# Performance work log

Measured on AMD Instinct MI355X. Metric: run time of the kernel, lower is better.

## Reference

```python
import jax, jax.numpy as jnp
import numpy as np

EPS = 0.01       # l2-normalize epsilon
BN_EPS = 0.001   # batchnorm epsilon

def _l2norm(u):
    # tf.math.l2_normalize over axis=-2: x / sqrt(max(sum(x^2), eps))
    sq = jnp.sum(u * u, axis=-2, keepdims=True)
    return u / jnp.sqrt(jnp.maximum(sq, EPS))

def _dotprod(t, u):
    # einsum '...ij,...ik->...jk' contracting spatial axis, then flatten (C,C)->C*C
    d = jnp.einsum('bndi,bndj->bnij', t, _l2norm(u))
    return d.reshape(d.shape[0], d.shape[1], -1)

def _bn(x, gamma, beta):
    # inference-mode BN with moving_mean=0, moving_var=1 (fresh init)
    return gamma * (x / jnp.sqrt(1.0 + BN_EPS)) + beta

def setup_inputs() -> dict:
    key = jax.random.key(0)
    ks = jax.random.split(key, 9)
    B, N, D, C, BAS, U_IN, U_EQ = 8, 1024, 3, 64, 16, 512, 64
    F = 2 * C * C  # 8192 invariant features (2 input heads)
    t1 = jax.random.normal(ks[0], (B, N, D, C), dtype=jnp.float32)
    t2 = jax.random.normal(ks[1], (B, N, D, C), dtype=jnp.float32)
    u1 = jax.random.normal(ks[2], (B, N, D, C), dtype=jnp.float32)
    u2 = jax.random.normal(ks[3], (B, N, D, C), dtype=jnp.float32)
    V1 = jax.random.normal(ks[4], (B, N, D, BAS), dtype=jnp.float32)
    V2 = jax.random.normal(ks[5], (B, N, D, BAS), dtype=jnp.float32)
    W_inv = jax.random.normal(ks[6], (F, U_IN), dtype=jnp.float32) * 0.02
    b_inv = jnp.zeros((U_IN,), dtype=jnp.float32)
    g_inv = jnp.ones((U_IN,), dtype=jnp.float32)
    be_inv = jnp.zeros((U_IN,), dtype=jnp.float32)
    # two equivariant heads, each Dense(units=U_EQ*BAS)
    W_eq = jax.random.normal(ks[7], (2, F, U_EQ * BAS), dtype=jnp.float32) * 0.02
    b_eq = jnp.zeros((2, U_EQ * BAS), dtype=jnp.float32)
    g_eq = jnp.ones((2, U_EQ * BAS), dtype=jnp.float32)
    be_eq = jnp.zeros((2, U_EQ * BAS), dtype=jnp.float32)
    return {"t1": t1, "t2": t2, "u1": u1, "u2": u2, "V1": V1, "V2": V2,
            "W_inv": W_inv, "b_inv": b_inv, "g_inv": g_inv, "be_inv": be_inv,
            "W_eq": W_eq, "b_eq": b_eq, "g_eq": g_eq, "be_eq": be_eq}

def reference(t1, t2, u1, u2, V1, V2, W_inv, b_inv, g_inv, be_inv,
              W_eq, b_eq, g_eq, be_eq):
    # invariant features: concatenated flattened Gram blocks of the two heads
    feats = jnp.concatenate([_dotprod(t1, u1), _dotprod(t2, u2)], axis=-1)  # (B,N,F)
    # invariant branch: Dense -> BN -> ReLU
    invar = jax.nn.relu(_bn(feats @ W_inv + b_inv, g_inv, be_inv))  # (B,N,U_IN)
    # equivariant branch per head: Dense -> BN -> ReLU -> reshape -> basis recombine
    bas = V1.shape[-1]
    u_eq = W_eq.shape[-1] // bas
    eq_outs = []
    for l, V in enumerate((V1, V2)):
        wl = jax.nn.relu(_bn(feats @ W_eq[l] + b_eq[l], g_eq[l], be_eq[l]))
        wl = wl.reshape(wl.shape[0], wl.shape[1], u_eq, bas)  # (B,N,units,basis)
        # einsum '...ij,...mj->...mi': combine basis vectors -> (B,N,3,units)
        eq_outs.append(jnp.einsum('bnij,bnmj->bnmi', wl, V))
    eqvar = jnp.concatenate(eq_outs, axis=-1)  # (B,N,3,2*units)
    return invar, eqvar
```

## Files before the change

### kernel.cpp

```cpp
#include <hip/hip_runtime.h>
#include <hip/hip_bf16.h>

#define BROWS 8192
#define DDIM 3
#define CDIM 64
#define KF 8192
#define NINV 512
#define NEQ 1024
#define NTOT 2560
#define BAS 16
#define UEQ 64


typedef float f32x4 __attribute__((ext_vector_type(4)));
typedef __bf16 bf16x8_t __attribute__((ext_vector_type(8)));
typedef __bf16 bf16x4_t __attribute__((ext_vector_type(4)));

__device__ __forceinline__ void async_copy16(const void* g, void* l) {
    __builtin_amdgcn_global_load_lds(
        (__attribute__((address_space(1))) void*)(g),
        (__attribute__((address_space(3))) void*)(l), 16, 0, 0);
}

#define FROWS 16
#define FSTRIDE 196

__global__ __launch_bounds__(256) void feats_kernel(
    const float* __restrict__ t1, const float* __restrict__ t2,
    const float* __restrict__ u1, const float* __restrict__ u2,
    __hip_bfloat16* __restrict__ feats)
{
    __shared__ float sT1[FROWS * FSTRIDE];
    __shared__ float sT2[FROWS * FSTRIDE];
    __shared__ float sU1[FROWS * FSTRIDE];
    __shared__ float sU2[FROWS * FSTRIDE];

    const int tid = threadIdx.x;
    const int r0  = blockIdx.x * FROWS;

    #pragma unroll
    for (int k = 0; k < 12; ++k) {
        const int item = k * 256 + tid;
        const int r = item / 192, c = item - r * 192;
        const size_t g = (size_t)(r0 + r) * 192 + c;
        const int l = r * FSTRIDE + c;
        sT1[l] = t1[g];
        sT2[l] = t2[g];
        sU1[l] = u1[g];
        sU2[l] = u2[g];
    }
    __syncthreads();

    #pragma unroll
    for (int k = 0; k < 8; ++k) {
        const int item = k * 256 + tid;
        const int r = item >> 7, rem = item & 127;
        const int h = rem >> 6, c = rem & 63;
        float* U = (h ? sU2 : sU1) + r * FSTRIDE;
        float sq = U[c] * U[c] + U[64 + c] * U[64 + c] + U[128 + c] * U[128 + c];
        float s = 1.0f / sqrtf(fmaxf(sq, 0.01f));
        U[c] *= s; U[64 + c] *= s; U[128 + c] *= s;
    }
    __syncthreads();

    const int w       = tid >> 6;
    const int lane    = tid & 63;
    const int r_local = lane >> 2;
    const int p       = lane & 3;
    const int mb      = r0 >> 8;
    const int rloc0   = r0 & 255;
    const int rloc    = rloc0 + r_local;
    const int lc      = (p - (rloc >> 1)) & 3;
    const float* Tarr = (w >= 2 ? sT2 : sT1) + r_local * FSTRIDE;
    const float* Uarr = (w >= 2 ? sU2 : sU1) + r_local * FSTRIDE;

    char* dst = (char*)feats + (((size_t)(mb * 256 + w * 64)) << 14)
              + rloc0 * 64 + lane * 16;

    #pragma unroll 4
    for (int it = 0; it < 64; ++it) {
        const int kt = w * 64 + it;
        const int i  = (kt >> 1) & 63;
        const int jh = (kt & 1) * 32;
        const int j0 = jh + lc * 8;
        const float ti0 = Tarr[i], ti1 = Tarr[64 + i], ti2 = Tarr[128 + i];
        bf16x8_t vv;
        #pragma unroll
        for (int half = 0; half < 2; ++half) {
            const int j = j0 + half * 4;
            const float4 u0 = *reinterpret_cast<const float4*>(Uarr + j);
            const float4 u1_ = *reinterpret_cast<const float4*>(Uarr + 64 + j);
            const float4 u2_ = *reinterpret_cast<const float4*>(Uarr + 128 + j);
            vv[half * 4 + 0] = (__bf16)(ti0 * u0.x + ti1 * u1_.x + ti2 * u2_.x);
            vv[half * 4 + 1] = (__bf16)(ti0 * u0.y + ti1 * u1_.y + ti2 * u2_.y);
            vv[half * 4 + 2] = (__bf16)(ti0 * u0.z + ti1 * u1_.z + ti2 * u2_.z);
            vv[half * 4 + 3] = (__bf16)(ti0 * u0.w + ti1 * u1_.w + ti2 * u2_.w);
        }
        *reinterpret_cast<bf16x8_t*>(dst) = vv;
        dst += 16384;
    }
}

__global__ __launch_bounds__(256) void wt_kernel(
    const float* __restrict__ W_inv, const float* __restrict__ W_eq,
    __hip_bfloat16* __restrict__ WT)
{
    __shared__ float tile[64][33];
    const int tid = threadIdx.x;
    const int n0 = blockIdx.x * 32;
    const int k0 = blockIdx.y * 64;

    const float* src; int ldn, nl0;
    if (n0 < NINV)            { src = W_inv;                       ldn = NINV; nl0 = n0; }
    else if (n0 < NINV + NEQ) { src = W_eq;                        ldn = NEQ;  nl0 = n0 - NINV; }
    else                      { src = W_eq + (size_t)KF * NEQ;     ldn = NEQ;  nl0 = n0 - NINV - NEQ; }

    {
        const int tx = tid & 31;
        const int ty = tid >> 5;
        #pragma unroll
        for (int i = 0; i < 8; ++i) {
            const int kl = ty + i * 8;
            tile[kl][tx] = src[(size_t)(k0 + kl) * ldn + nl0 + tx];
        }
    }
    __syncthreads();

    const int kt_l = tid >> 7;
    const int rem  = tid & 127;
    const int n_l  = rem >> 2;
    const int p    = rem & 3;

    const int n    = n0 + n_l;
    const int nb   = n / 320, rloc = n - nb * 320;
    const int kt_g = (k0 >> 5) + kt_l;
    const int lc   = (p - (rloc >> 1)) & 3;

    bf16x8_t v;
    #pragma unroll
    for (int e = 0; e < 8; ++e)
        v[e] = (__bf16)tile[kt_l * 32 + lc * 8 + e][n_l];

    char* dst = (char*)WT + ((size_t)(nb * 256 + kt_g)) * 20480
              + rloc * 64 + p * 16;
    *reinterpret_cast<bf16x8_t*>(dst) = v;
}

#define BM 128
#define BN 160
#define BK 32
#define ATILE 16384
#define BTILE 20480
#define AHALF 8192
#define BHALF 10240

__global__ __launch_bounds__(512, 4) void gemm_kernel(
    const __hip_bfloat16* __restrict__ A,
    const __hip_bfloat16* __restrict__ BT,
    const float* __restrict__ b_inv, const float* __restrict__ g_inv,
    const float* __restrict__ be_inv,
    const float* __restrict__ b_eq,  const float* __restrict__ g_eq,
    const float* __restrict__ be_eq,
    float* __restrict__ out_inv,
    float* __restrict__ Yeq)
{
    __shared__ alignas(16) __hip_bfloat16 AsBuf[4][BM * BK];
    __shared__ alignas(16) __hip_bfloat16 BsBuf[4][BN * BK];

    const int tid  = threadIdx.x;
    const int wave = tid >> 6;
    const int lane = tid & 63;
    const bool loWave = wave < 2;

    const int b    = blockIdx.x;
    const int xcd  = b & 7;
    const int slot = b >> 3;
    const int N    = slot & 15;
    const int M    = xcd * 8 + (slot >> 4);
    const int n0   = N * BN;
    const int m0   = M * BM;

    const char* pA = (const char*)A  + (size_t)(M >> 1) * 256 * ATILE
                   + (size_t)(M & 1) * AHALF;
    const char* pB = (const char*)BT + (size_t)(N >> 1) * 256 * BTILE
                   + (size_t)(N & 1) * BHALF;

    const int off16 = tid * 16;

    const int chnk = (((lane >> 4) + ((lane & 15) >> 1)) & 3) * 8;
    const int wm = (wave & 3) * 32;
    const int wn = (wave >> 2) * 80;
    const int l15 = lane & 15;

    f32x4 acc[2][5] = {};

#define ISSUE(bufi, t)                                                        \
    do {                                                                      \
        async_copy16(pA + (size_t)(t) * ATILE + off16,                        \
                     (char*)&AsBuf[bufi][0] + off16);                         \
        async_copy16(pB + (size_t)(t) * BTILE + off16,                        \
                     (char*)&BsBuf[bufi][0] + off16);                         \
        if (loWave)                                                           \
            async_copy16(pB + (size_t)(t) * BTILE + 8192 + off16,             \
                         (char*)&BsBuf[bufi][0] + 8192 + off16);              \
    } while (0)

#define COMPUTE(bufi)                                                         \
    do {                                                                      \
        bf16x8_t a_[2];                                                       \
        _Pragma("unroll")                                                     \
        for (int mt = 0; mt < 2; ++mt)                                        \
            a_[mt] = *reinterpret_cast<const bf16x8_t*>(                      \
                &AsBuf[bufi][(wm + mt * 16 + l15) * BK + chnk]);              \
        _Pragma("unroll")                                                     \
        for (int nt = 0; nt < 5; ++nt) {                                      \
            bf16x8_t b_ = *reinterpret_cast<const bf16x8_t*>(                 \
                &BsBuf[bufi][(wn + nt * 16 + l15) * BK + chnk]);              \
            _Pragma("unroll")                                                 \
            for (int mt = 0; mt < 2; ++mt)                                    \
                acc[mt][nt] = __builtin_amdgcn_mfma_f32_16x16x32_bf16(        \
                    a_[mt], b_, acc[mt][nt], 0, 0, 0);                        \
        }                                                                     \
    } while (0)

#define WAITAB(na, nb_)                                                       \
    do {                                                                      \
        if (loWave) asm volatile("s_waitcnt vmcnt(" #na ")" ::: "memory");    \
        else        asm volatile("s_waitcnt vmcnt(" #nb_ ")" ::: "memory");   \
    } while (0)

#define MPHASE(b0, b1, t)                                                     \
    do {                                                                      \
        WAITAB(6, 4);                                                         \
        __builtin_amdgcn_s_barrier();                                         \
        asm volatile("" ::: "memory");                                        \
        COMPUTE(b0);                                                          \
        asm volatile("" ::: "memory");                                        \
        COMPUTE(b1);                                                          \
        asm volatile("" ::: "memory");                                        \
        __builtin_amdgcn_s_barrier();                                         \
        ISSUE(b0, t + 4);                                                     \
        ISSUE(b1, t + 5);                                                     \
    } while (0)

    ISSUE(0, 0);
    ISSUE(1, 1);
    ISSUE(2, 2);
    ISSUE(3, 3);

    for (int i = 0; i < 63; ++i) {
        const int t = i * 4;
        MPHASE(0, 1, t);
        MPHASE(2, 3, t + 2);
    }
    WAITAB(6, 4);
    __builtin_amdgcn_s_barrier();
    asm volatile("" ::: "memory");
    COMPUTE(0);
    asm volatile("" ::: "memory");
    COMPUTE(1);
    asm volatile("" ::: "memory");
    __builtin_amdgcn_s_barrier();

    asm volatile("s_waitcnt vmcnt(0)" ::: "memory");
    __builtin_amdgcn_s_barrier();
    asm volatile("" ::: "memory");
    COMPUTE(2);
    asm volatile("" ::: "memory");
    COMPUTE(3);

    const float RSQ = 0.9995003746877732f;
    #pragma unroll
    for (int nt = 0; nt < 5; ++nt) {
        const int gn = n0 + wn + nt * 16 + l15;
        float bbp, gg, bep;
        if (gn < NINV) {
            bbp = b_inv[gn]; gg = g_inv[gn]; bep = be_inv[gn];
        } else {
            const int e = gn - NINV, hh = e >> 10, nl = e & 1023;
            bbp = b_eq[hh * NEQ + nl]; gg = g_eq[hh * NEQ + nl]; bep = be_eq[hh * NEQ + nl];
        }
        gg *= RSQ;
        #pragma unroll
        for (int mt = 0; mt < 2; ++mt) {
            const int gmb = m0 + wm + mt * 16 + ((lane >> 4) << 2);
            #pragma unroll
            for (int rr = 0; rr < 4; ++rr) {
                float y = fmaxf(gg * (acc[mt][nt][rr] + bbp) + bep, 0.0f);
                const size_t gm = gmb + rr;
                if (gn < NINV) out_inv[gm * NINV + gn] = y;
                else           Yeq[gm * 2048 + (gn - NINV)] = y;
            }
        }
    }
#undef MPHASE
#undef WAITAB
#undef COMPUTE
#undef ISSUE
}

__global__ __launch_bounds__(128) void eqcomb_kernel(
    const float* __restrict__ Yeq,
    const float* __restrict__ V1, const float* __restrict__ V2,
    float* __restrict__ out_eq)
{
    const int row = blockIdx.x;
    const int tid = threadIdx.x;
    __shared__ float sV[2][DDIM][BAS];
    if (tid < 96) {
        const int h = tid / 48, rem = tid % 48;
        const float* V = h ? V2 : V1;
        sV[h][rem / BAS][rem % BAS] = V[(size_t)row * (DDIM * BAS) + rem];
    }
    __syncthreads();
    const int l = tid >> 6, u = tid & 63;
    const float4* y4 = reinterpret_cast<const float4*>(
        Yeq + (size_t)row * 2048 + l * 1024 + u * BAS);
    float a0 = 0.f, a1 = 0.f, a2 = 0.f;
    #pragma unroll
    for (int q = 0; q < 4; ++q) {
        float4 w = y4[q];
        const float* v0 = sV[l][0] + q * 4;
        const float* v1 = sV[l][1] + q * 4;
        const float* v2 = sV[l][2] + q * 4;
        a0 += w.x * v0[0] + w.y * v0[1] + w.z * v0[2] + w.w * v0[3];
        a1 += w.x * v1[0] + w.y * v1[1] + w.z * v1[2] + w.w * v1[3];
        a2 += w.x * v2[0] + w.y * v2[1] + w.z * v2[2] + w.w * v2[3];
    }
    float* o = out_eq + (size_t)row * (DDIM * 128);
    o[0 * 128 + l * 64 + u] = a0;
    o[1 * 128 + l * 64 + u] = a1;
    o[2 * 128 + l * 64 + u] = a2;
}

extern "C" void kernel_launch(void* const* d_in, const int* in_sizes, int n_in,
                              void* d_out, int out_size, void* d_ws, size_t ws_size,
                              hipStream_t stream) {
    const float* t1    = (const float*)d_in[0];
    const float* t2    = (const float*)d_in[1];
    const float* u1    = (const float*)d_in[2];
    const float* u2    = (const float*)d_in[3];
    const float* V1    = (const float*)d_in[4];
    const float* V2    = (const float*)d_in[5];
    const float* W_inv = (const float*)d_in[6];
    const float* b_inv = (const float*)d_in[7];
    const float* g_inv = (const float*)d_in[8];
    const float* be_inv= (const float*)d_in[9];
    const float* W_eq  = (const float*)d_in[10];
    const float* b_eq  = (const float*)d_in[11];
    const float* g_eq  = (const float*)d_in[12];
    const float* be_eq = (const float*)d_in[13];
    float* out = (float*)d_out;

    char* ws = (char*)d_ws;
    __hip_bfloat16* feats = (__hip_bfloat16*)(ws);
    __hip_bfloat16* WT    = (__hip_bfloat16*)(ws + 134217728);
    float*          Yeq   = (float*)(ws + 176160768);

    float* out_inv = out;
    float* out_eq  = out + (size_t)BROWS * NINV;

    hipLaunchKernelGGL(feats_kernel, dim3(BROWS / FROWS), dim3(256), 0, stream,
                       t1, t2, u1, u2, feats);
    hipLaunchKernelGGL(wt_kernel, dim3(NTOT / 32, KF / 64), dim3(256), 0, stream,
                       W_inv, W_eq, WT);
    hipLaunchKernelGGL(gemm_kernel, dim3((NTOT / BN) * (BROWS / BM)), dim3(512), 0, stream,
                       feats, WT, b_inv, g_inv, be_inv, b_eq, g_eq, be_eq,
                       out_inv, Yeq);
    hipLaunchKernelGGL(eqcomb_kernel, dim3(BROWS), dim3(128), 0, stream,
                       Yeq, V1, V2, out_eq);
}
```

Before: 523.9 us.

## Shrink GEMM N-tile to 128 with triple-buffered single-phase pipeline

Reduces the GEMM block tile from 128x160 to 128x128, which gives 20 N-tiles and 1280 blocks, and switches the 4-stage double-phase pipeline to a 3-stage single-phase one. B tiles are now read from the existing 320-row packed layout through split pointers, because a 128-row slice can cross a packing boundary. The smaller LDS footprint and accumulator set allow a higher occupancy hint (6 blocks per CU). In exchange, each block does less work per loaded A tile, so A traffic rises, and there are more barriers per k-step.

After: 553.3 us. 1.06x slower.

```diff
diff --git a/kernel.cpp b/kernel.cpp
--- a/kernel.cpp
+++ b/kernel.cpp
@@ -147,14 +147,13 @@
 }
 
 #define BM 128
-#define BN 160
+#define BN 128
 #define BK 32
 #define ATILE 16384
 #define BTILE 20480
 #define AHALF 8192
-#define BHALF 10240
-
-__global__ __launch_bounds__(512, 4) void gemm_kernel(
+
+__global__ __launch_bounds__(512, 6) void gemm_kernel(
     const __hip_bfloat16* __restrict__ A,
     const __hip_bfloat16* __restrict__ BT,
     const float* __restrict__ b_inv, const float* __restrict__ g_inv,
@@ -164,45 +163,47 @@
     float* __restrict__ out_inv,
     float* __restrict__ Yeq)
 {
-    __shared__ alignas(16) __hip_bfloat16 AsBuf[4][BM * BK];
-    __shared__ alignas(16) __hip_bfloat16 BsBuf[4][BN * BK];
+    __shared__ alignas(16) __hip_bfloat16 AsBuf[3][BM * BK];
+    __shared__ alignas(16) __hip_bfloat16 BsBuf[3][BN * BK];
 
     const int tid  = threadIdx.x;
     const int wave = tid >> 6;
     const int lane = tid & 63;
-    const bool loWave = wave < 2;
 
     const int b    = blockIdx.x;
     const int xcd  = b & 7;
     const int slot = b >> 3;
-    const int N    = slot & 15;
-    const int M    = xcd * 8 + (slot >> 4);
+    const int N    = slot % 20;
+    const int M    = xcd * 8 + slot / 20;
     const int n0   = N * BN;
     const int m0   = M * BM;
 
-    const char* pA = (const char*)A  + (size_t)(M >> 1) * 256 * ATILE
+    const char* pA = (const char*)A + (size_t)(M >> 1) * 256 * ATILE
                    + (size_t)(M & 1) * AHALF;
-    const char* pB = (const char*)BT + (size_t)(N >> 1) * 256 * BTILE
-                   + (size_t)(N & 1) * BHALF;
+
+    const int gr0 = N * BN;
+    const int pt0 = gr0 / 320;
+    const int off0 = gr0 - pt0 * 320;
+    const int sB   = (off0 == 256) ? 4096 : 8192;
+    const char* pB0 = (const char*)BT + ((size_t)pt0 * 256) * BTILE + off0 * 64;
+    const char* pB1 = (const char*)BT + ((size_t)(pt0 + 1) * 256) * BTILE - sB;
 
     const int off16 = tid * 16;
+    const char* pBs = (off16 < sB) ? pB0 : pB1;
 
     const int chnk = (((lane >> 4) + ((lane & 15) >> 1)) & 3) * 8;
     const int wm = (wave & 3) * 32;
-    const int wn = (wave >> 2) * 80;
+    const int wn = (wave >> 2) * 64;
     const int l15 = lane & 15;
 
-    f32x4 acc[2][5] = {};
+    f32x4 acc[2][4] = {};
 
 #define ISSUE(bufi, t)                                                        \
     do {                                                                      \
-        async_copy16(pA + (size_t)(t) * ATILE + off16,                        \
+        async_copy16(pA  + (size_t)(t) * ATILE + off16,                       \
                      (char*)&AsBuf[bufi][0] + off16);                         \
-        async_copy16(pB + (size_t)(t) * BTILE + off16,                        \
+        async_copy16(pBs + (size_t)(t) * BTILE + off16,                       \
                      (char*)&BsBuf[bufi][0] + off16);                         \
-        if (loWave)                                                           \
-            async_copy16(pB + (size_t)(t) * BTILE + 8192 + off16,             \
-                         (char*)&BsBuf[bufi][0] + 8192 + off16);              \
     } while (0)
 
 #define COMPUTE(bufi)                                                         \
@@ -213,7 +214,7 @@
             a_[mt] = *reinterpret_cast<const bf16x8_t*>(                      \
                 &AsBuf[bufi][(wm + mt * 16 + l15) * BK + chnk]);              \
         _Pragma("unroll")                                                     \
-        for (int nt = 0; nt < 5; ++nt) {                                      \
+        for (int nt = 0; nt < 4; ++nt) {                                      \
             bf16x8_t b_ = *reinterpret_cast<const bf16x8_t*>(                 \
                 &BsBuf[bufi][(wn + nt * 16 + l15) * BK + chnk]);              \
             _Pragma("unroll")                                                 \
@@ -223,55 +224,59 @@
         }                                                                     \
     } while (0)
 
-#define WAITAB(na, nb_)                                                       \
+#define WAITN(n) asm volatile("s_waitcnt vmcnt(" #n ")" ::: "memory")
+
+#define PHASE(bufi, t)                                                        \
     do {                                                                      \
-        if (loWave) asm volatile("s_waitcnt vmcnt(" #na ")" ::: "memory");    \
-        else        asm volatile("s_waitcnt vmcnt(" #nb_ ")" ::: "memory");   \
-    } while (0)
-
-#define MPHASE(b0, b1, t)                                                     \
-    do {                                                                      \
-        WAITAB(6, 4);                                                         \
+        WAITN(4);                                                             \
         __builtin_amdgcn_s_barrier();                                         \
         asm volatile("" ::: "memory");                                        \
-        COMPUTE(b0);                                                          \
-        asm volatile("" ::: "memory");                                        \
-        COMPUTE(b1);                                                          \
+        COMPUTE(bufi);                                                        \
         asm volatile("" ::: "memory");                                        \
         __builtin_amdgcn_s_barrier();                                         \
-        ISSUE(b0, t + 4);                                                     \
-        ISSUE(b1, t + 5);                                                     \
+        ISSUE(bufi, t);                                                       \
     } while (0)
 
     ISSUE(0, 0);
     ISSUE(1, 1);
     ISSUE(2, 2);
-    ISSUE(3, 3);
-
-    for (int i = 0; i < 63; ++i) {
-        const int t = i * 4;
-        MPHASE(0, 1, t);
-        MPHASE(2, 3, t + 2);
-    }
-    WAITAB(6, 4);
+
+    for (int i = 0; i < 84; ++i) {
+        const int t = i * 3;
+        PHASE(0, t + 3);
+        PHASE(1, t + 4);
+        PHASE(2, t + 5);
+    }
+    WAITN(4);
     __builtin_amdgcn_s_barrier();
     asm volatile("" ::: "memory");
     COMPUTE(0);
     asm volatile("" ::: "memory");
+    __builtin_amdgcn_s_barrier();
+    ISSUE(0, 255);
+
+    WAITN(4);
+    __builtin_amdgcn_s_barrier();
+    asm volatile("" ::: "memory");
     COMPUTE(1);
     asm volatile("" ::: "memory");
     __builtin_amdgcn_s_barrier();
 
-    asm volatile("s_waitcnt vmcnt(0)" ::: "memory");
+    WAITN(2);
     __builtin_amdgcn_s_barrier();
     asm volatile("" ::: "memory");
     COMPUTE(2);
     asm volatile("" ::: "memory");
-    COMPUTE(3);
+    __builtin_amdgcn_s_barrier();
+
+    WAITN(0);
+    __builtin_amdgcn_s_barrier();
+    asm volatile("" ::: "memory");
+    COMPUTE(0);
 
     const float RSQ = 0.9995003746877732f;
     #pragma unroll
-    for (int nt = 0; nt < 5; ++nt) {
+    for (int nt = 0; nt < 4; ++nt) {
         const int gn = n0 + wn + nt * 16 + l15;
         float bbp, gg, bep;
         if (gn < NINV) {
@@ -293,8 +298,8 @@
             }
         }
     }
-#undef MPHASE
-#undef WAITAB
+#undef PHASE
+#undef WAITN
 #undef COMPUTE
 #undef ISSUE
 }
```
